# Kernel optimization log

Measured on AMD Instinct MI355X. Metric: run time of the kernel, lower is better.

## Reference

```python
import jax, jax.numpy as jnp
import numpy as np

N_NODES = 100000


def leaky(x):
    return jax.nn.leaky_relu(x, negative_slope=0.01)


def gcn_conv(h, W, b, src, dst, n_nodes):
    """PyG GCNConv: add self-loops, symmetric deg^{-1/2} normalization, scatter-add."""
    h = h @ W  # [N, out]
    deg = jax.ops.segment_sum(jnp.ones_like(dst, dtype=h.dtype), dst, num_segments=n_nodes) + 1.0  # +1 self-loop
    dinv = jax.lax.rsqrt(deg)  # deg >= 1 always
    norm = dinv[src] * dinv[dst]  # [E]
    msg = h[src] * norm[:, None]  # gather + scale, [E, out]
    agg = jax.ops.segment_sum(msg, dst, num_segments=n_nodes)
    agg = agg + h * (dinv * dinv)[:, None]  # self-loop message
    return agg + b


def setup_inputs() -> dict:
    key = jax.random.key(0)
    ks = jax.random.split(key, 16)
    num_teams = 100000
    n_edges = 5000000
    n_matches = 1000000
    x = jax.random.randint(ks[0], (N_NODES, 1), 0, num_teams)
    edge_index = jax.random.randint(ks[1], (2, n_edges), 0, N_NODES)
    home = jax.random.randint(ks[2], (n_matches,), 0, N_NODES)
    away = jax.random.randint(ks[3], (n_matches,), 0, N_NODES)
    emb = jax.random.normal(ks[4], (num_teams, 3), dtype=jnp.float32)
    W1 = jax.random.normal(ks[5], (3, 16), dtype=jnp.float32) * (1.0 / np.sqrt(3))
    b1 = jnp.zeros((16,), dtype=jnp.float32)
    W2 = jax.random.normal(ks[6], (16, 3), dtype=jnp.float32) * 0.25
    b2 = jnp.zeros((3,), dtype=jnp.float32)
    lw1 = jax.random.normal(ks[7], (6, 16), dtype=jnp.float32) * (1.0 / np.sqrt(6))
    lb1 = jnp.zeros((16,), dtype=jnp.float32)
    lw2 = jax.random.normal(ks[8], (16, 6), dtype=jnp.float32) * 0.25
    lb2 = jnp.zeros((6,), dtype=jnp.float32)
    lw3 = jax.random.normal(ks[9], (6, 3), dtype=jnp.float32) * (1.0 / np.sqrt(6))
    lb3 = jnp.zeros((3,), dtype=jnp.float32)
    return dict(x=x, edge_index=edge_index, home=home, away=away, emb=emb,
                W1=W1, b1=b1, W2=W2, b2=b2,
                lw1=lw1, lb1=lb1, lw2=lw2, lb2=lb2, lw3=lw3, lb3=lb3)


def reference(x, edge_index, home, away, emb, W1, b1, W2, b2, lw1, lb1, lw2, lb2, lw3, lb3):
    src, dst = edge_index[0], edge_index[1]
    h = emb[x[:, 0]]  # embedding lookup + squeeze(1) -> [N, 3]
    h = leaky(gcn_conv(h, W1, b1, src, dst, N_NODES))  # [N, 16]
    h = leaky(gcn_conv(h, W2, b2, src, dst, N_NODES))  # [N, 3]
    z = jnp.concatenate([h[home], h[away]], axis=-1)  # [M, 6]
    z = leaky(z @ lw1 + lb1)
    z = leaky(z @ lw2 + lb2)
    z = leaky(z @ lw3 + lb3)
    return z.reshape(-1, 3)
```

## Files before the change

### kernel.cpp

```cpp
#include <hip/hip_runtime.h>

typedef unsigned int u32;
typedef unsigned char u8;

static __device__ __forceinline__ float leaky(float v) {
    return v >= 0.0f ? v : 0.01f * v;
}

#define P1_CHUNK 8192
#define P1T 1024
#define NBK 512
#define CAPB 16384
#define ASPLIT 8
#define S1F 8388608.0f
#define S2F 2097152.0f

__global__ __launch_bounds__(1024) void k_p1scatterA(
        const int* __restrict__ src, const int* __restrict__ dst,
        int* __restrict__ cur, u32* __restrict__ bkt, int nE) {
    __shared__ int sc[NBK];
    __shared__ int loff[NBK];
    __shared__ int gb[NBK];
    __shared__ int lcur[NBK];
    __shared__ int wsum[8];
    __shared__ u32 pay[P1_CHUNK];
    __shared__ u8 bb[P1_CHUNK];
    int t = threadIdx.x;
    if (t < NBK) sc[t] = 0;
    __syncthreads();
    int base = blockIdx.x * P1_CHUNK;
    int lim = min(P1_CHUNK, nE - base);
    if (lim == P1_CHUNK) {
        const int4* p = (const int4*)(dst + base);
        for (int i = t; i < P1_CHUNK / 4; i += P1T) {
            int4 v = p[i];
            atomicAdd(&sc[v.x >> 8], 1);
            atomicAdd(&sc[v.y >> 8], 1);
            atomicAdd(&sc[v.z >> 8], 1);
            atomicAdd(&sc[v.w >> 8], 1);
        }
    } else {
        for (int i = t; i < lim; i += P1T)
            atomicAdd(&sc[dst[base + i] >> 8], 1);
    }
    __syncthreads();
    if (t < NBK) {
        int c = sc[t];
        int lane = t & 63;
        int incl = c;
#pragma unroll
        for (int o = 1; o < 64; o <<= 1) {
            int xv = __shfl_up(incl, o);
            if (lane >= o) incl += xv;
        }
        if (lane == 63) wsum[t >> 6] = incl;
        sc[t] = incl;
    }
    __syncthreads();
    if (t == 0) {
        int run = 0;
#pragma unroll
        for (int k = 0; k < 8; ++k) { int v = wsum[k]; wsum[k] = run; run += v; }
    }
    __syncthreads();
    if (t < NBK) {
        int c;
        {
            int inclw = sc[t];
            int prev = (t & 63) ? sc[t - 1] : 0;
            c = inclw - prev;
            int excl = prev + wsum[t >> 6];
            loff[t] = excl;
            lcur[t] = excl;
            gb[t] = (t << 14) + ((c > 0) ? atomicAdd(&cur[t], c) : 0);
        }
    }
    __syncthreads();
    int loff256 = loff[256];
    int n4 = lim >> 2;
    const int4* d4p = (const int4*)(dst + base);
    const int4* s4p = (const int4*)(src + base);
    for (int i = t; i < n4; i += P1T) {
        int4 d4 = d4p[i];
        int4 s4 = s4p[i];
        int b, r;
        b = d4.x >> 8; r = atomicAdd(&lcur[b], 1);
        pay[r] = (u32)(((d4.x & 255) << 17) | s4.x); bb[r] = (u8)b;
        b = d4.y >> 8; r = atomicAdd(&lcur[b], 1);
        pay[r] = (u32)(((d4.y & 255) << 17) | s4.y); bb[r] = (u8)b;
        b = d4.z >> 8; r = atomicAdd(&lcur[b], 1);
        pay[r] = (u32)(((d4.z & 255) << 17) | s4.z); bb[r] = (u8)b;
        b = d4.w >> 8; r = atomicAdd(&lcur[b], 1);
        pay[r] = (u32)(((d4.w & 255) << 17) | s4.w); bb[r] = (u8)b;
    }
    for (int i = (n4 << 2) + t; i < lim; i += P1T) {
        int d = dst[base + i], s = src[base + i];
        int b = d >> 8;
        int r = atomicAdd(&lcur[b], 1);
        pay[r] = (u32)(((d & 255) << 17) | s);
        bb[r] = (u8)b;
    }
    __syncthreads();
    for (int i = t; i < lim; i += P1T) {
        int b = (int)bb[i] | ((i >= loff256) ? 256 : 0);
        bkt[gb[b] + (i - loff[b])] = pay[i];
    }
}

__global__ __launch_bounds__(1024) void k_cnt1F(
        const u32* __restrict__ bkt, const int* __restrict__ cur,
        const int* __restrict__ x, const float* __restrict__ emb,
        float* __restrict__ dinv, float4* __restrict__ hd0, int nN) {
    __shared__ int h[256];
    int t = threadIdx.x, b = blockIdx.x;
    if (t < 256) h[t] = 0;
    __syncthreads();
    int base = b << 14;
    int end = base + cur[b];
    int vend = base + ((end - base) & ~3);
    for (int i = base + t * 4; i < vend; i += 1024 * 4) {
        uint4 v = *(const uint4*)&bkt[i];
        atomicAdd(&h[v.x >> 17], 1);
        atomicAdd(&h[v.y >> 17], 1);
        atomicAdd(&h[v.z >> 17], 1);
        atomicAdd(&h[v.w >> 17], 1);
    }
    if (vend + t < end) atomicAdd(&h[bkt[vend + t] >> 17], 1);
    __syncthreads();
    if (t < 256) {
        int d = b * 256 + t;
        if (d < nN) {
            float di = rsqrtf((float)h[t] + 1.0f);
            dinv[d] = di;
            int xi = x[d] * 3;
            hd0[d] = make_float4(emb[xi] * di, emb[xi + 1] * di,
                                 emb[xi + 2] * di, 0.f);
        }
    }
}

__global__ __launch_bounds__(256) void k_aggIF(
        const u32* __restrict__ bkt, const int* __restrict__ cur,
        const float4* __restrict__ tab, float* __restrict__ pacc,
        float scale, float inv_scale) {
    __shared__ int acc[768];
    int t = threadIdx.x;
    int blk = blockIdx.x, b = blk >> 3, s = blk & 7;
    int base = b << 14;
    int sz = cur[b];
    int chunk = (sz + ASPLIT - 1) / ASPLIT;
    int st = min(base + s * chunk, base + sz);
    int en = min(st + chunk, base + sz);
    acc[t] = 0; acc[t + 256] = 0; acc[t + 512] = 0;
    __syncthreads();
    int a0 = min((st + 3) & ~3, en);
    if (st + t < a0) {
        u32 v = bkt[st + t];
        float4 h = tab[v & 0x1FFFFu];
        int bin = (int)(v >> 17) * 3;
        atomicAdd(&acc[bin + 0], __float2int_rn(h.x * scale));
        atomicAdd(&acc[bin + 1], __float2int_rn(h.y * scale));
        atomicAdd(&acc[bin + 2], __float2int_rn(h.z * scale));
    }
    int vend = a0 + ((en - a0) & ~3);
    for (int i = a0 + t * 4; i < vend; i += 256 * 4) {
        uint4 v = *(const uint4*)&bkt[i];
        float4 h0 = tab[v.x & 0x1FFFFu];
        float4 h1 = tab[v.y & 0x1FFFFu];
        float4 h2 = tab[v.z & 0x1FFFFu];
        float4 h3 = tab[v.w & 0x1FFFFu];
        int b0 = (int)(v.x >> 17) * 3, b1 = (int)(v.y >> 17) * 3;
        int b2 = (int)(v.z >> 17) * 3, b3 = (int)(v.w >> 17) * 3;
        atomicAdd(&acc[b0 + 0], __float2int_rn(h0.x * scale));
        atomicAdd(&acc[b0 + 1], __float2int_rn(h0.y * scale));
        atomicAdd(&acc[b0 + 2], __float2int_rn(h0.z * scale));
        atomicAdd(&acc[b1 + 0], __float2int_rn(h1.x * scale));
        atomicAdd(&acc[b1 + 1], __float2int_rn(h1.y * scale));
        atomicAdd(&acc[b1 + 2], __float2int_rn(h1.z * scale));
        atomicAdd(&acc[b2 + 0], __float2int_rn(h2.x * scale));
        atomicAdd(&acc[b2 + 1], __float2int_rn(h2.y * scale));
        atomicAdd(&acc[b2 + 2], __float2int_rn(h2.z * scale));
        atomicAdd(&acc[b3 + 0], __float2int_rn(h3.x * scale));
        atomicAdd(&acc[b3 + 1], __float2int_rn(h3.y * scale));
        atomicAdd(&acc[b3 + 2], __float2int_rn(h3.z * scale));
    }
    if (vend + t < en) {
        u32 v = bkt[vend + t];
        float4 h = tab[v & 0x1FFFFu];
        int bin = (int)(v >> 17) * 3;
        atomicAdd(&acc[bin + 0], __float2int_rn(h.x * scale));
        atomicAdd(&acc[bin + 1], __float2int_rn(h.y * scale));
        atomicAdd(&acc[bin + 2], __float2int_rn(h.z * scale));
    }
    __syncthreads();
    float* p = pacc + (size_t)blk * 768;
    p[t]       = (float)acc[t * 3 + 0] * inv_scale;
    p[t + 256] = (float)acc[t * 3 + 1] * inv_scale;
    p[t + 512] = (float)acc[t * 3 + 2] * inv_scale;
}

__global__ void k_fin1(const float* __restrict__ pacc, const float* __restrict__ dinv,
                       const float4* __restrict__ hd0,
                       const float* __restrict__ W1, const float* __restrict__ b1,
                       const float* __restrict__ W2,
                       float4* __restrict__ hd2, int nN) {
    int d = blockIdx.x * blockDim.x + threadIdx.x;
    if (d >= nN) return;
    int b = d >> 8, q = d & 255;
    float s0 = 0.f, s1 = 0.f, s2 = 0.f;
#pragma unroll
    for (int s = 0; s < ASPLIT; ++s) {
        const float* p = pacc + (size_t)(b * ASPLIT + s) * 768;
        s0 += p[q]; s1 += p[q + 256]; s2 += p[q + 512];
    }
    float di = dinv[d];
    float4 self = hd0[d];
    float a0 = di * (s0 + self.x);
    float a1 = di * (s1 + self.y);
    float a2 = di * (s2 + self.z);
    float o0 = 0.f, o1 = 0.f, o2 = 0.f;
#pragma unroll
    for (int k = 0; k < 16; ++k) {
        float p = leaky(a0 * W1[k] + a1 * W1[16 + k] + a2 * W1[32 + k] + b1[k]);
        o0 += p * W2[k * 3 + 0];
        o1 += p * W2[k * 3 + 1];
        o2 += p * W2[k * 3 + 2];
    }
    hd2[d] = make_float4(o0 * di, o1 * di, o2 * di, 0.f);
}

__global__ void k_fin2(const float* __restrict__ pacc, const float* __restrict__ dinv,
                       const float4* __restrict__ hd2, const float* __restrict__ b2,
                       float4* __restrict__ h2, int nN) {
    int d = blockIdx.x * blockDim.x + threadIdx.x;
    if (d >= nN) return;
    int b = d >> 8, q = d & 255;
    float s0 = 0.f, s1 = 0.f, s2 = 0.f;
#pragma unroll
    for (int s = 0; s < ASPLIT; ++s) {
        const float* p = pacc + (size_t)(b * ASPLIT + s) * 768;
        s0 += p[q]; s1 += p[q + 256]; s2 += p[q + 512];
    }
    float di = dinv[d];
    float4 self = hd2[d];
    h2[d] = make_float4(leaky(di * (s0 + self.x) + b2[0]),
                        leaky(di * (s1 + self.y) + b2[1]),
                        leaky(di * (s2 + self.z) + b2[2]), 0.f);
}

__global__ __launch_bounds__(256) void k_mlp4v(
        const int* __restrict__ home, const int* __restrict__ away,
        const float4* __restrict__ h2,
        const float* __restrict__ lw1, const float* __restrict__ lb1,
        const float* __restrict__ lw2, const float* __restrict__ lb2,
        const float* __restrict__ lw3, const float* __restrict__ lb3,
        float* __restrict__ out, int nM) {
    __shared__ float s[235];
    int t = threadIdx.x;
    if (t < 96)       s[t] = lw1[t];
    else if (t < 112) s[t] = lb1[t - 96];
    else if (t < 208) s[t] = lw2[t - 112];
    else if (t < 214) s[t] = lb2[t - 208];
    else if (t < 232) s[t] = lw3[t - 214];
    else if (t < 235) s[t] = lb3[t - 232];
    __syncthreads();
    const float* sw1 = s;        const float* sb1 = s + 96;
    const float* sw2 = s + 112;  const float* sb2 = s + 208;
    const float* sw3 = s + 214;  const float* sb3 = s + 232;
    int i = blockIdx.x * blockDim.x + threadIdx.x;
    int m0 = i * 4;
    if (m0 >= nM) return;
    float res[12];
    int nq = min(4, nM - m0);
    int hidx[4], aidx[4];
    if (nq == 4) {
        int4 hv = *(const int4*)&home[m0];
        int4 av = *(const int4*)&away[m0];
        hidx[0] = hv.x; hidx[1] = hv.y; hidx[2] = hv.z; hidx[3] = hv.w;
        aidx[0] = av.x; aidx[1] = av.y; aidx[2] = av.z; aidx[3] = av.w;
    } else {
        for (int j = 0; j < nq; ++j) { hidx[j] = home[m0 + j]; aidx[j] = away[m0 + j]; }
    }
    for (int j = 0; j < nq; ++j) {
        float4 zh = h2[hidx[j]];
        float4 za = h2[aidx[j]];
        float z[6] = {zh.x, zh.y, zh.z, za.x, za.y, za.z};
        float t1[16];
#pragma unroll
        for (int k = 0; k < 16; ++k) {
            float p = sb1[k];
#pragma unroll
            for (int q = 0; q < 6; ++q) p += z[q] * sw1[q * 16 + k];
            t1[k] = leaky(p);
        }
        float t2[6];
#pragma unroll
        for (int k = 0; k < 6; ++k) {
            float p = sb2[k];
#pragma unroll
            for (int q = 0; q < 16; ++q) p += t1[q] * sw2[q * 6 + k];
            t2[k] = leaky(p);
        }
#pragma unroll
        for (int k = 0; k < 3; ++k) {
            float p = sb3[k];
#pragma unroll
            for (int q = 0; q < 6; ++q) p += t2[q] * sw3[q * 3 + k];
            res[j * 3 + k] = leaky(p);
        }
    }
    if (nq == 4) {
        float4* o4 = (float4*)&out[m0 * 3];
        o4[0] = make_float4(res[0], res[1], res[2], res[3]);
        o4[1] = make_float4(res[4], res[5], res[6], res[7]);
        o4[2] = make_float4(res[8], res[9], res[10], res[11]);
    } else {
        for (int j = 0; j < nq * 3; ++j) out[m0 * 3 + j] = res[j];
    }
}

__global__ void f_deg(const int* __restrict__ dst, float* __restrict__ deg, int nE) {
    int e = blockIdx.x * blockDim.x + threadIdx.x;
    if (e < nE) atomicAdd(&deg[dst[e]], 1.0f);
}
__global__ void f_hd0(const int* __restrict__ x, const float* __restrict__ emb,
                      float* __restrict__ dinv, float4* __restrict__ hd0, int nN) {
    int i = blockIdx.x * blockDim.x + threadIdx.x;
    if (i >= nN) return;
    float di = rsqrtf(dinv[i] + 1.0f);
    dinv[i] = di;
    int xi = x[i] * 3;
    hd0[i] = make_float4(emb[xi] * di, emb[xi + 1] * di, emb[xi + 2] * di, 0.f);
}
__global__ void f_scatter(const int* __restrict__ src, const int* __restrict__ dst,
                          const float4* __restrict__ tab, float* __restrict__ agg, int nE) {
    int e = blockIdx.x * blockDim.x + threadIdx.x;
    if (e >= nE) return;
    int s = src[e], d = dst[e];
    float4 v = tab[s];
    atomicAdd(&agg[d * 3 + 0], v.x);
    atomicAdd(&agg[d * 3 + 1], v.y);
    atomicAdd(&agg[d * 3 + 2], v.z);
}
__global__ void f_fin1(const float* __restrict__ agg, const float* __restrict__ dinv,
                       const float4* __restrict__ hd0,
                       const float* __restrict__ W1, const float* __restrict__ b1,
                       const float* __restrict__ W2, float4* __restrict__ hd2, int nN) {
    int d = blockIdx.x * blockDim.x + threadIdx.x;
    if (d >= nN) return;
    float di = dinv[d];
    float4 self = hd0[d];
    float a0 = di * (agg[d * 3 + 0] + self.x);
    float a1 = di * (agg[d * 3 + 1] + self.y);
    float a2 = di * (agg[d * 3 + 2] + self.z);
    float o0 = 0.f, o1 = 0.f, o2 = 0.f;
#pragma unroll
    for (int k = 0; k < 16; ++k) {
        float p = leaky(a0 * W1[k] + a1 * W1[16 + k] + a2 * W1[32 + k] + b1[k]);
        o0 += p * W2[k * 3 + 0];
        o1 += p * W2[k * 3 + 1];
        o2 += p * W2[k * 3 + 2];
    }
    hd2[d] = make_float4(o0 * di, o1 * di, o2 * di, 0.f);
}
__global__ void f_fin2(const float* __restrict__ agg, const float* __restrict__ dinv,
                       const float4* __restrict__ hd2, const float* __restrict__ b2,
                       float4* __restrict__ h2, int nN) {
    int d = blockIdx.x * blockDim.x + threadIdx.x;
    if (d >= nN) return;
    float di = dinv[d];
    float4 self = hd2[d];
    h2[d] = make_float4(leaky(di * (agg[d * 3 + 0] + self.x) + b2[0]),
                        leaky(di * (agg[d * 3 + 1] + self.y) + b2[1]),
                        leaky(di * (agg[d * 3 + 2] + self.z) + b2[2]), 0.f);
}

extern "C" void kernel_launch(void* const* d_in, const int* in_sizes, int n_in,
                              void* d_out, int out_size, void* d_ws, size_t ws_size,
                              hipStream_t stream) {
    const int*   x    = (const int*)d_in[0];
    const int*   ei   = (const int*)d_in[1];
    const int*   home = (const int*)d_in[2];
    const int*   away = (const int*)d_in[3];
    const float* emb  = (const float*)d_in[4];
    const float* W1   = (const float*)d_in[5];
    const float* b1   = (const float*)d_in[6];
    const float* W2   = (const float*)d_in[7];
    const float* b2   = (const float*)d_in[8];
    const float* lw1  = (const float*)d_in[9];
    const float* lb1  = (const float*)d_in[10];
    const float* lw2  = (const float*)d_in[11];
    const float* lb2  = (const float*)d_in[12];
    const float* lw3  = (const float*)d_in[13];
    const float* lb3  = (const float*)d_in[14];
    float* out = (float*)d_out;

    const int nN = in_sizes[0];
    const int nE = in_sizes[1] / 2;
    const int nM = in_sizes[2];
    const int* src = ei;
    const int* dst = ei + nE;
    const int B = 256;

    const int nb1 = (nE + P1_CHUNK - 1) / P1_CHUNK;
    const size_t paccN = (size_t)NBK * ASPLIT * 768;
    const size_t bktN = (size_t)NBK * CAPB;

    size_t need = (size_t)3 * nN * 16 + bktN * 4 + paccN * 4 +
                  (size_t)nN * 4 + NBK * 4;

    double mean_b = (double)nE * 256.0 / (double)nN;
    double sig_b = sqrt(mean_b);
    bool cap_ok = (mean_b + 10.0 * sig_b) < (double)CAPB;

    if (nN <= NBK * 256 && ws_size >= need && cap_ok) {
        char* w = (char*)d_ws;
        float4* hd0 = (float4*)w;                 w += (size_t)nN * 16;
        float4* hd2 = (float4*)w;                 w += (size_t)nN * 16;
        float4* h2  = (float4*)w;                 w += (size_t)nN * 16;
        u32* bkt  = (u32*)w;                      w += bktN * 4;
        float* pacc = (float*)w;                  w += paccN * 4;
        float* dinv = (float*)w;                  w += (size_t)nN * 4;
        int* cur  = (int*)w;

        hipMemsetAsync(cur, 0, NBK * sizeof(int), stream);
        k_p1scatterA<<<nb1, P1T, 0, stream>>>(src, dst, cur, bkt, nE);
        k_cnt1F<<<NBK, 1024, 0, stream>>>(bkt, cur, x, emb, dinv, hd0, nN);
        k_aggIF<<<NBK * ASPLIT, 256, 0, stream>>>(bkt, cur, hd0, pacc,
                                                  S1F, 1.0f / S1F);
        k_fin1<<<(nN + B - 1) / B, B, 0, stream>>>(pacc, dinv, hd0, W1, b1, W2,
                                                   hd2, nN);
        k_aggIF<<<NBK * ASPLIT, 256, 0, stream>>>(bkt, cur, hd2, pacc,
                                                  S2F, 1.0f / S2F);
        k_fin2<<<(nN + B - 1) / B, B, 0, stream>>>(pacc, dinv, hd2, b2, h2, nN);
        int nQuads = (nM + 3) / 4;
        k_mlp4v<<<(nQuads + B - 1) / B, B, 0, stream>>>(home, away, h2,
                                                        lw1, lb1, lw2, lb2,
                                                        lw3, lb3, out, nM);
    } else {
        char* w = (char*)d_ws;
        float4* hd0 = (float4*)w;                 w += (size_t)nN * 16;
        float4* hd2 = (float4*)w;                 w += (size_t)nN * 16;
        float4* h2  = (float4*)w;                 w += (size_t)nN * 16;
        float* agg  = (float*)w;                  w += (size_t)3 * nN * 4;
        float* dinv = (float*)w;

        hipMemsetAsync(dinv, 0, (size_t)nN * sizeof(float), stream);
        hipMemsetAsync(agg, 0, (size_t)3 * nN * sizeof(float), stream);
        f_deg<<<(nE + B - 1) / B, B, 0, stream>>>(dst, dinv, nE);
        f_hd0<<<(nN + B - 1) / B, B, 0, stream>>>(x, emb, dinv, hd0, nN);
        f_scatter<<<(nE + B - 1) / B, B, 0, stream>>>(src, dst, hd0, agg, nE);
        f_fin1<<<(nN + B - 1) / B, B, 0, stream>>>(agg, dinv, hd0, W1, b1, W2, hd2, nN);
        hipMemsetAsync(agg, 0, (size_t)3 * nN * sizeof(float), stream);
        f_scatter<<<(nE + B - 1) / B, B, 0, stream>>>(src, dst, hd2, agg, nE);
        f_fin2<<<(nN + B - 1) / B, B, 0, stream>>>(agg, dinv, hd2, b2, h2, nN);
        int nQuads = (nM + 3) / 4;
        k_mlp4v<<<(nQuads + B - 1) / B, B, 0, stream>>>(home, away, h2,
                                                        lw1, lb1, lw2, lb2,
                                                        lw3, lb3, out, nM);
    }
}
```

Baseline: 128.7 us.

## Fuse per-bucket aggregation with finalize kernels, one 1024-thread block per bucket

Replaces the split aggregation (8 sub-blocks of 256 threads per bucket writing partial sums to global memory, followed by separate finalize kernels) with one 1024-thread block per bucket that accumulates in shared memory and applies the layer transform directly. This removes the partial-sum buffer traffic and two kernel launches per layer. In exchange, only 512 blocks are launched instead of 4096, so there is less parallelism and load balance across CUs, and 1024 threads contend on the same 768 shared-memory atomic counters.

```diff
diff --git a/kernel.cpp b/kernel.cpp
--- a/kernel.cpp
+++ b/kernel.cpp
@@ -11,7 +11,6 @@
 #define P1T 1024
 #define NBK 512
 #define CAPB 16384
-#define ASPLIT 8
 #define S1F 8388608.0f
 #define S2F 2097152.0f
 
@@ -64,16 +63,13 @@
     }
     __syncthreads();
     if (t < NBK) {
-        int c;
-        {
-            int inclw = sc[t];
-            int prev = (t & 63) ? sc[t - 1] : 0;
-            c = inclw - prev;
-            int excl = prev + wsum[t >> 6];
-            loff[t] = excl;
-            lcur[t] = excl;
-            gb[t] = (t << 14) + ((c > 0) ? atomicAdd(&cur[t], c) : 0);
-        }
+        int inclw = sc[t];
+        int prev = (t & 63) ? sc[t - 1] : 0;
+        int c = inclw - prev;
+        int excl = prev + wsum[t >> 6];
+        loff[t] = excl;
+        lcur[t] = excl;
+        gb[t] = (t << 14) + ((c > 0) ? atomicAdd(&cur[t], c) : 0);
     }
     __syncthreads();
     int loff256 = loff[256];
@@ -139,113 +135,128 @@
     }
 }
 
-__global__ __launch_bounds__(256) void k_aggIF(
+__global__ __launch_bounds__(1024) void k_aggF1(
         const u32* __restrict__ bkt, const int* __restrict__ cur,
-        const float4* __restrict__ tab, float* __restrict__ pacc,
-        float scale, float inv_scale) {
+        const float4* __restrict__ hd0, const float* __restrict__ dinv,
+        const float* __restrict__ W1, const float* __restrict__ b1,
+        const float* __restrict__ W2,
+        float4* __restrict__ hd2, int nN) {
     __shared__ int acc[768];
-    int t = threadIdx.x;
-    int blk = blockIdx.x, b = blk >> 3, s = blk & 7;
+    int t = threadIdx.x, b = blockIdx.x;
+    if (t < 768) acc[t] = 0;
+    __syncthreads();
     int base = b << 14;
-    int sz = cur[b];
-    int chunk = (sz + ASPLIT - 1) / ASPLIT;
-    int st = min(base + s * chunk, base + sz);
-    int en = min(st + chunk, base + sz);
-    acc[t] = 0; acc[t + 256] = 0; acc[t + 512] = 0;
-    __syncthreads();
-    int a0 = min((st + 3) & ~3, en);
-    if (st + t < a0) {
-        u32 v = bkt[st + t];
-        float4 h = tab[v & 0x1FFFFu];
+    int end = base + cur[b];
+    int vend = base + ((end - base) & ~3);
+    for (int i = base + t * 4; i < vend; i += 1024 * 4) {
+        uint4 v = *(const uint4*)&bkt[i];
+        float4 h0 = hd0[v.x & 0x1FFFFu];
+        float4 h1 = hd0[v.y & 0x1FFFFu];
+        float4 h2v = hd0[v.z & 0x1FFFFu];
+        float4 h3 = hd0[v.w & 0x1FFFFu];
+        int b0 = (int)(v.x >> 17) * 3, b1i = (int)(v.y >> 17) * 3;
+        int b2i = (int)(v.z >> 17) * 3, b3 = (int)(v.w >> 17) * 3;
+        atomicAdd(&acc[b0 + 0], __float2int_rn(h0.x * S1F));
+        atomicAdd(&acc[b0 + 1], __float2int_rn(h0.y * S1F));
+        atomicAdd(&acc[b0 + 2], __float2int_rn(h0.z * S1F));
+        atomicAdd(&acc[b1i + 0], __float2int_rn(h1.x * S1F));
+        atomicAdd(&acc[b1i + 1], __float2int_rn(h1.y * S1F));
+        atomicAdd(&acc[b1i + 2], __float2int_rn(h1.z * S1F));
+        atomicAdd(&acc[b2i + 0], __float2int_rn(h2v.x * S1F));
+        atomicAdd(&acc[b2i + 1], __float2int_rn(h2v.y * S1F));
+        atomicAdd(&acc[b2i + 2], __float2int_rn(h2v.z * S1F));
+        atomicAdd(&acc[b3 + 0], __float2int_rn(h3.x * S1F));
+        atomicAdd(&acc[b3 + 1], __float2int_rn(h3.y * S1F));
+        atomicAdd(&acc[b3 + 2], __float2int_rn(h3.z * S1F));
+    }
+    if (vend + t < end) {
+        u32 v = bkt[vend + t];
+        float4 h = hd0[v & 0x1FFFFu];
         int bin = (int)(v >> 17) * 3;
-        atomicAdd(&acc[bin + 0], __float2int_rn(h.x * scale));
-        atomicAdd(&acc[bin + 1], __float2int_rn(h.y * scale));
-        atomicAdd(&acc[bin + 2], __float2int_rn(h.z * scale));
-    }
-    int vend = a0 + ((en - a0) & ~3);
-    for (int i = a0 + t * 4; i < vend; i += 256 * 4) {
+        atomicAdd(&acc[bin + 0], __float2int_rn(h.x * S1F));
+        atomicAdd(&acc[bin + 1], __float2int_rn(h.y * S1F));
+        atomicAdd(&acc[bin + 2], __float2int_rn(h.z * S1F));
+    }
+    __syncthreads();
+    if (t < 256) {
+        int d = b * 256 + t;
+        if (d < nN) {
+            float s0 = (float)acc[t * 3 + 0] * (1.0f / S1F);
+            float s1 = (float)acc[t * 3 + 1] * (1.0f / S1F);
+            float s2 = (float)acc[t * 3 + 2] * (1.0f / S1F);
+            float di = dinv[d];
+            float4 self = hd0[d];
+            float a0 = di * (s0 + self.x);
+            float a1 = di * (s1 + self.y);
+            float a2 = di * (s2 + self.z);
+            float o0 = 0.f, o1 = 0.f, o2 = 0.f;
+#pragma unroll
+            for (int k = 0; k < 16; ++k) {
+                float p = leaky(a0 * W1[k] + a1 * W1[16 + k] + a2 * W1[32 + k] + b1[k]);
+                o0 += p * W2[k * 3 + 0];
+                o1 += p * W2[k * 3 + 1];
+                o2 += p * W2[k * 3 + 2];
+            }
+            hd2[d] = make_float4(o0 * di, o1 * di, o2 * di, 0.f);
+        }
+    }
+}
+
+__global__ __launch_bounds__(1024) void k_aggF2(
+        const u32* __restrict__ bkt, const int* __restrict__ cur,
+        const float4* __restrict__ hd2, const float* __restrict__ dinv,
+        const float* __restrict__ b2,
+        float4* __restrict__ h2, int nN) {
+    __shared__ int acc[768];
+    int t = threadIdx.x, b = blockIdx.x;
+    if (t < 768) acc[t] = 0;
+    __syncthreads();
+    int base = b << 14;
+    int end = base + cur[b];
+    int vend = base + ((end - base) & ~3);
+    for (int i = base + t * 4; i < vend; i += 1024 * 4) {
         uint4 v = *(const uint4*)&bkt[i];
-        float4 h0 = tab[v.x & 0x1FFFFu];
-        float4 h1 = tab[v.y & 0x1FFFFu];
-        float4 h2 = tab[v.z & 0x1FFFFu];
-        float4 h3 = tab[v.w & 0x1FFFFu];
-        int b0 = (int)(v.x >> 17) * 3, b1 = (int)(v.y >> 17) * 3;
-        int b2 = (int)(v.z >> 17) * 3, b3 = (int)(v.w >> 17) * 3;
-        atomicAdd(&acc[b0 + 0], __float2int_rn(h0.x * scale));
-        atomicAdd(&acc[b0 + 1], __float2int_rn(h0.y * scale));
-        atomicAdd(&acc[b0 + 2], __float2int_rn(h0.z * scale));
-        atomicAdd(&acc[b1 + 0], __float2int_rn(h1.x * scale));
-        atomicAdd(&acc[b1 + 1], __float2int_rn(h1.y * scale));
-        atomicAdd(&acc[b1 + 2], __float2int_rn(h1.z * scale));
-        atomicAdd(&acc[b2 + 0], __float2int_rn(h2.x * scale));
-        atomicAdd(&acc[b2 + 1], __float2int_rn(h2.y * scale));
-        atomicAdd(&acc[b2 + 2], __float2int_rn(h2.z * scale));
-        atomicAdd(&acc[b3 + 0], __float2int_rn(h3.x * scale));
-        atomicAdd(&acc[b3 + 1], __float2int_rn(h3.y * scale));
-        atomicAdd(&acc[b3 + 2], __float2int_rn(h3.z * scale));
-    }
-    if (vend + t < en) {
+        float4 h0 = hd2[v.x & 0x1FFFFu];
+        float4 h1 = hd2[v.y & 0x1FFFFu];
+        float4 h2v = hd2[v.z & 0x1FFFFu];
+        float4 h3 = hd2[v.w & 0x1FFFFu];
+        int b0 = (int)(v.x >> 17) * 3, b1i = (int)(v.y >> 17) * 3;
+        int b2i = (int)(v.z >> 17) * 3, b3 = (int)(v.w >> 17) * 3;
+        atomicAdd(&acc[b0 + 0], __float2int_rn(h0.x * S2F));
+        atomicAdd(&acc[b0 + 1], __float2int_rn(h0.y * S2F));
+        atomicAdd(&acc[b0 + 2], __float2int_rn(h0.z * S2F));
+        atomicAdd(&acc[b1i + 0], __float2int_rn(h1.x * S2F));
+        atomicAdd(&acc[b1i + 1], __float2int_rn(h1.y * S2F));
+        atomicAdd(&acc[b1i + 2], __float2int_rn(h1.z * S2F));
+        atomicAdd(&acc[b2i + 0], __float2int_rn(h2v.x * S2F));
+        atomicAdd(&acc[b2i + 1], __float2int_rn(h2v.y * S2F));
+        atomicAdd(&acc[b2i + 2], __float2int_rn(h2v.z * S2F));
+        atomicAdd(&acc[b3 + 0], __float2int_rn(h3.x * S2F));
+        atomicAdd(&acc[b3 + 1], __float2int_rn(h3.y * S2F));
+        atomicAdd(&acc[b3 + 2], __float2int_rn(h3.z * S2F));
+    }
+    if (vend + t < end) {
         u32 v = bkt[vend + t];
-        float4 h = tab[v & 0x1FFFFu];
+        float4 h = hd2[v & 0x1FFFFu];
         int bin = (int)(v >> 17) * 3;
-        atomicAdd(&acc[bin + 0], __float2int_rn(h.x * scale));
-        atomicAdd(&acc[bin + 1], __float2int_rn(h.y * scale));
-        atomicAdd(&acc[bin + 2], __float2int_rn(h.z * scale));
-    }
-    __syncthreads();
-    float* p = pacc + (size_t)blk * 768;
-    p[t]       = (float)acc[t * 3 + 0] * inv_scale;
-    p[t + 256] = (float)acc[t * 3 + 1] * inv_scale;
-    p[t + 512] = (float)acc[t * 3 + 2] * inv_scale;
-}
-
-__global__ void k_fin1(const float* __restrict__ pacc, const float* __restrict__ dinv,
-                       const float4* __restrict__ hd0,
-                       const float* __restrict__ W1, const float* __restrict__ b1,
-                       const float* __restrict__ W2,
-                       float4* __restrict__ hd2, int nN) {
-    int d = blockIdx.x * blockDim.x + threadIdx.x;
-    if (d >= nN) return;
-    int b = d >> 8, q = d & 255;
-    float s0 = 0.f, s1 = 0.f, s2 = 0.f;
-#pragma unroll
-    for (int s = 0; s < ASPLIT; ++s) {
-        const float* p = pacc + (size_t)(b * ASPLIT + s) * 768;
-        s0 += p[q]; s1 += p[q + 256]; s2 += p[q + 512];
-    }
-    float di = dinv[d];
-    float4 self = hd0[d];
-    float a0 = di * (s0 + self.x);
-    float a1 = di * (s1 + self.y);
-    float a2 = di * (s2 + self.z);
-    float o0 = 0.f, o1 = 0.f, o2 = 0.f;
-#pragma unroll
-    for (int k = 0; k < 16; ++k) {
-        float p = leaky(a0 * W1[k] + a1 * W1[16 + k] + a2 * W1[32 + k] + b1[k]);
-        o0 += p * W2[k * 3 + 0];
-        o1 += p * W2[k * 3 + 1];
-        o2 += p * W2[k * 3 + 2];
-    }
-    hd2[d] = make_float4(o0 * di, o1 * di, o2 * di, 0.f);
-}
-
-__global__ void k_fin2(const float* __restrict__ pacc, const float* __restrict__ dinv,
-                       const float4* __restrict__ hd2, const float* __restrict__ b2,
-                       float4* __restrict__ h2, int nN) {
-    int d = blockIdx.x * blockDim.x + threadIdx.x;
-    if (d >= nN) return;
-    int b = d >> 8, q = d & 255;
-    float s0 = 0.f, s1 = 0.f, s2 = 0.f;
-#pragma unroll
-    for (int s = 0; s < ASPLIT; ++s) {
-        const float* p = pacc + (size_t)(b * ASPLIT + s) * 768;
-        s0 += p[q]; s1 += p[q + 256]; s2 += p[q + 512];
-    }
-    float di = dinv[d];
-    float4 self = hd2[d];
-    h2[d] = make_float4(leaky(di * (s0 + self.x) + b2[0]),
-                        leaky(di * (s1 + self.y) + b2[1]),
-                        leaky(di * (s2 + self.z) + b2[2]), 0.f);
+        atomicAdd(&acc[bin + 0], __float2int_rn(h.x * S2F));
+        atomicAdd(&acc[bin + 1], __float2int_rn(h.y * S2F));
+        atomicAdd(&acc[bin + 2], __float2int_rn(h.z * S2F));
+    }
+    __syncthreads();
+    if (t < 256) {
+        int d = b * 256 + t;
+        if (d < nN) {
+            float s0 = (float)acc[t * 3 + 0] * (1.0f / S2F);
+            float s1 = (float)acc[t * 3 + 1] * (1.0f / S2F);
+            float s2 = (float)acc[t * 3 + 2] * (1.0f / S2F);
+            float di = dinv[d];
+            float4 self = hd2[d];
+            h2[d] = make_float4(leaky(di * (s0 + self.x) + b2[0]),
+                                leaky(di * (s1 + self.y) + b2[1]),
+                                leaky(di * (s2 + self.z) + b2[2]), 0.f);
+        }
+    }
 }
 
 __global__ __launch_bounds__(256) void k_mlp4v(
@@ -403,11 +414,9 @@
     const int B = 256;
 
     const int nb1 = (nE + P1_CHUNK - 1) / P1_CHUNK;
-    const size_t paccN = (size_t)NBK * ASPLIT * 768;
     const size_t bktN = (size_t)NBK * CAPB;
 
-    size_t need = (size_t)3 * nN * 16 + bktN * 4 + paccN * 4 +
-                  (size_t)nN * 4 + NBK * 4;
+    size_t need = (size_t)3 * nN * 16 + bktN * 4 + (size_t)nN * 4 + NBK * 4;
 
     double mean_b = (double)nE * 256.0 / (double)nN;
     double sig_b = sqrt(mean_b);
@@ -419,20 +428,15 @@
         float4* hd2 = (float4*)w;                 w += (size_t)nN * 16;
         float4* h2  = (float4*)w;                 w += (size_t)nN * 16;
         u32* bkt  = (u32*)w;                      w += bktN * 4;
-        float* pacc = (float*)w;                  w += paccN * 4;
         float* dinv = (float*)w;                  w += (size_t)nN * 4;
         int* cur  = (int*)w;
 
         hipMemsetAsync(cur, 0, NBK * sizeof(int), stream);
         k_p1scatterA<<<nb1, P1T, 0, stream>>>(src, dst, cur, bkt, nE);
         k_cnt1F<<<NBK, 1024, 0, stream>>>(bkt, cur, x, emb, dinv, hd0, nN);
-        k_aggIF<<<NBK * ASPLIT, 256, 0, stream>>>(bkt, cur, hd0, pacc,
-                                                  S1F, 1.0f / S1F);
-        k_fin1<<<(nN + B - 1) / B, B, 0, stream>>>(pacc, dinv, hd0, W1, b1, W2,
-                                                   hd2, nN);
-        k_aggIF<<<NBK * ASPLIT, 256, 0, stream>>>(bkt, cur, hd2, pacc,
-                                                  S2F, 1.0f / S2F);
-        k_fin2<<<(nN + B - 1) / B, B, 0, stream>>>(pacc, dinv, hd2, b2, h2, nN);
+        k_aggF1<<<NBK, 1024, 0, stream>>>(bkt, cur, hd0, dinv, W1, b1, W2,
+                                          hd2, nN);
+        k_aggF2<<<NBK, 1024, 0, stream>>>(bkt, cur, hd2, dinv, b2, h2, nN);
         int nQuads = (nM + 3) / 4;
         k_mlp4v<<<(nQuads + B - 1) / B, B, 0, stream>>>(home, away, h2,
                                                         lw1, lb1, lw2, lb2,
```

After: 122.5 us. 1.05x faster.
